# Kernel optimization log

Hardware: AMD Instinct MI355X
Metric: run time of the kernel (lower is better)

## Reference

```python
import jax, jax.numpy as jnp
import numpy as np

D_MODEL = 512
NHEAD = 8
HEAD_DIM = D_MODEL // NHEAD
SEQ = 4096
BATCH = 2
BASE = 10000.0


def rope_cache(seq_len, dim):
    inv_freq = 1.0 / (BASE ** (jnp.arange(0, dim, 2, dtype=jnp.float32) / dim))
    t = jnp.arange(seq_len, dtype=jnp.float32)
    freqs = jnp.einsum('i,j->ij', t, inv_freq)          # [S, dim/2]
    emb = jnp.concatenate([freqs, freqs], axis=-1)       # [S, dim]
    return jnp.cos(emb), jnp.sin(emb)


def rotate_half(x):
    h = x.shape[-1] // 2
    return jnp.concatenate([-x[..., h:], x[..., :h]], axis=-1)


def setup_inputs() -> dict:
    key = jax.random.key(0)
    ks = jax.random.split(key, 9)
    s = 1.0 / np.sqrt(D_MODEL)
    x = jax.random.normal(ks[0], (BATCH, SEQ, D_MODEL), dtype=jnp.float32)
    Wq = jax.random.uniform(ks[1], (D_MODEL, D_MODEL), jnp.float32, -s, s)
    bq = jax.random.uniform(ks[2], (D_MODEL,), jnp.float32, -s, s)
    Wk = jax.random.uniform(ks[3], (D_MODEL, D_MODEL), jnp.float32, -s, s)
    bk = jax.random.uniform(ks[4], (D_MODEL,), jnp.float32, -s, s)
    Wv = jax.random.uniform(ks[5], (D_MODEL, D_MODEL), jnp.float32, -s, s)
    bv = jax.random.uniform(ks[6], (D_MODEL,), jnp.float32, -s, s)
    Wo = jax.random.uniform(ks[7], (D_MODEL, D_MODEL), jnp.float32, -s, s)
    bo = jax.random.uniform(ks[8], (D_MODEL,), jnp.float32, -s, s)
    # causal mask: True where attention is disallowed (j > i)
    mask = jnp.triu(jnp.ones((SEQ, SEQ), dtype=bool), k=1)
    return {"x": x, "mask": mask, "Wq": Wq, "bq": bq, "Wk": Wk, "bk": bk,
            "Wv": Wv, "bv": bv, "Wo": Wo, "bo": bo}


def reference(x, mask, Wq, bq, Wk, bk, Wv, bv, Wo, bo):
    B, S, _ = x.shape
    def proj(W, b):
        y = x @ W.T + b
        return y.reshape(B, S, NHEAD, HEAD_DIM).transpose(0, 2, 1, 3)  # [B,H,S,D]
    q = proj(Wq, bq)
    k = proj(Wk, bk)
    v = proj(Wv, bv)
    cos, sin = rope_cache(S, HEAD_DIM)                    # [S, D]
    cos = cos[None, None]; sin = sin[None, None]
    q = q * cos + rotate_half(q) * sin
    k = k * cos + rotate_half(k) * sin
    scale = HEAD_DIM ** -0.5
    attn = jnp.einsum('bhid,bhjd->bhij', q, k) * scale    # [B,H,S,S]
    attn = jnp.where(mask[None, None], -jnp.inf, attn)
    attn = jax.nn.softmax(attn, axis=-1)
    out = jnp.einsum('bhij,bhjd->bhid', attn, v)          # [B,H,S,D]
    out = out.transpose(0, 2, 1, 3).reshape(B, S, D_MODEL)
    return out @ Wo.T + bo
```

## Files before the change

### kernel.cpp

```cpp
#include <hip/hip_runtime.h>
#include <hip/hip_bf16.h>

#define SEQLEN 4096
#define DMODEL 512
#define NHEADS 8

typedef short short8 __attribute__((ext_vector_type(8)));
typedef float f32x4  __attribute__((ext_vector_type(4)));
typedef float f32x16 __attribute__((ext_vector_type(16)));

__device__ __forceinline__ unsigned short f2bf(float f) {
    union { float f; unsigned u; } v; v.f = f;
    unsigned r = v.u + 0x7fffu + ((v.u >> 16) & 1u);
    return (unsigned short)(r >> 16);
}
__device__ __forceinline__ float exp2v(float x) {
    float r; asm("v_exp_f32 %0, %1" : "=v"(r) : "v"(x)); return r;
}
__device__ __forceinline__ unsigned cvtpk(float lo, float hi) {
    unsigned r; asm("v_cvt_pk_bf16_f32 %0, %1, %2" : "=v"(r) : "v"(lo), "v"(hi)); return r;
}
__device__ __forceinline__ void gload16(const void* g, void* l) {
    __builtin_amdgcn_global_load_lds(
        (const __attribute__((address_space(1))) void*)g,
        (__attribute__((address_space(3))) void*)l, 16, 0, 0);
}

__global__ __launch_bounds__(256)
void prep_kernel(const float* __restrict__ x,
                 const float* __restrict__ Wq, const float* __restrict__ Wk,
                 const float* __restrict__ Wv, const float* __restrict__ Wo,
                 unsigned short* __restrict__ xb, unsigned short* __restrict__ Wcat,
                 float* __restrict__ ct, float* __restrict__ st) {
    const int gid = blockIdx.x, tid = threadIdx.x;
    if (gid < 4096) {
        int i = gid * 1024 + tid * 4;
        float4 v = *reinterpret_cast<const float4*>(x + i);
        ushort4 o; o.x = f2bf(v.x); o.y = f2bf(v.y); o.z = f2bf(v.z); o.w = f2bf(v.w);
        *reinterpret_cast<ushort4*>(xb + i) = o;
    } else if (gid < 5120) {
        int i = (gid - 4096) * 1024 + tid * 4;
        int z = i >> 18;
        const float* W = (z == 0) ? Wq : (z == 1) ? Wk : (z == 2) ? Wv : Wo;
        int j = i & 262143;
        float4 v = *reinterpret_cast<const float4*>(W + j);
        ushort4 o; o.x = f2bf(v.x); o.y = f2bf(v.y); o.z = f2bf(v.z); o.w = f2bf(v.w);
        *reinterpret_cast<ushort4*>(Wcat + i) = o;
    } else {
        int idx = (gid - 5120) * 256 + tid;
        int s = idx >> 5, f = idx & 31;
        float inv = powf(10000.0f, -(float)f * (1.0f / 32.0f));
        float a = (float)s * inv;
        ct[idx] = cosf(a); st[idx] = sinf(a);
    }
}

template<int MODE>
__global__ __launch_bounds__(256)
void gemm_kernel(const unsigned short* __restrict__ A,
                 const unsigned short* __restrict__ W,
                 const float* __restrict__ bq,
                 const float* __restrict__ bk,
                 const float* __restrict__ bv,
                 const float* __restrict__ ctab,
                 const float* __restrict__ stab,
                 unsigned short* __restrict__ Qb,
                 unsigned short* __restrict__ Kb,
                 unsigned short* __restrict__ Vb,
                 float* __restrict__ Fout)
{
    constexpr int K = 512;
    constexpr int NT = (MODE == 0) ? 12 : 4;
    __shared__ __align__(16) unsigned short a_sh[2][128 * 32];
    __shared__ __align__(16) unsigned short b_sh[2][128 * 32];

    const int bid = blockIdx.x;
    const int bm = bid / NT, bn = bid % NT;
    const int tid = threadIdx.x;
    const int w = tid >> 6, l = tid & 63;
    const int g = l >> 4, l15 = l & 15;
    const int wr = w >> 1, wc = w & 1;

    const int sr0 = tid >> 2;
    const int swzc = (tid & 3) ^ ((sr0 >> 1) & 3);
    const unsigned wbase = (unsigned)(tid & 0xC0) * 16;
    const unsigned short* arow = A + (size_t)(bm * 128 + sr0) * K + swzc * 8;
    const unsigned short* brow = W + (size_t)(bn * 128 + sr0) * K + swzc * 8;

    f32x4 acc[4][4];
    #pragma unroll
    for (int p = 0; p < 4; ++p)
        #pragma unroll
        for (int q = 0; q < 4; ++q)
            acc[p][q] = (f32x4){0.f, 0.f, 0.f, 0.f};

    auto stage = [&](int buf, int k0) {
        char* ab = (char*)a_sh[buf];
        char* bb2 = (char*)b_sh[buf];
        #pragma unroll
        for (int rr = 0; rr < 2; ++rr)
            gload16(arow + (size_t)rr * 64 * K + k0, ab + rr * 4096 + wbase);
        #pragma unroll
        for (int rr = 0; rr < 2; ++rr)
            gload16(brow + (size_t)rr * 64 * K + k0, bb2 + rr * 4096 + wbase);
    };

    stage(0, 0);
    asm volatile("s_waitcnt vmcnt(0)" ::: "memory");
    __syncthreads();

    for (int ks = 0; ks < 16; ++ks) {
        const int buf = ks & 1;
        if (ks < 15) stage(buf ^ 1, (ks + 1) * 32);

        const char* ab = (const char*)a_sh[buf];
        const char* bb2 = (const char*)b_sh[buf];
        short8 af[4], bf[4];
        #pragma unroll
        for (int mt = 0; mt < 4; ++mt) {
            int r = wr * 64 + mt * 16 + l15;
            int ofs = (r * 64 + g * 16) ^ (((r >> 1) & 3) << 4);
            af[mt] = *reinterpret_cast<const short8*>(ab + ofs);
        }
        #pragma unroll
        for (int nt = 0; nt < 4; ++nt) {
            int r = wc * 64 + nt * 16 + l15;
            int ofs = (r * 64 + g * 16) ^ (((r >> 1) & 3) << 4);
            bf[nt] = *reinterpret_cast<const short8*>(bb2 + ofs);
        }
        __builtin_amdgcn_s_setprio(1);
        #pragma unroll
        for (int mt = 0; mt < 4; ++mt)
            #pragma unroll
            for (int nt = 0; nt < 4; ++nt)
                acc[mt][nt] = __builtin_amdgcn_mfma_f32_16x16x32_bf16(af[mt], bf[nt], acc[mt][nt], 0, 0, 0);
        __builtin_amdgcn_s_setprio(0);

        asm volatile("s_waitcnt vmcnt(0)" ::: "memory");
        __syncthreads();
    }

    const int m_base = bm * 128 + wr * 64;

    if (MODE == 1) {
        const int n_base = bn * 128 + wc * 64;
        #pragma unroll
        for (int mt = 0; mt < 4; ++mt)
            for (int nt = 0; nt < 4; ++nt) {
                int n = n_base + nt * 16 + l15;
                float bb = bq[n];
                #pragma unroll
                for (int i = 0; i < 4; ++i) {
                    int m = m_base + mt * 16 + g * 4 + i;
                    Fout[(size_t)m * 512 + n] = acc[mt][nt][i] + bb;
                }
            }
    } else {
        const int z = bn >> 2;
        const int nc0 = (bn & 3) * 128 + wc * 64;
        const float* bias = (z == 0) ? bq : (z == 1) ? bk : bv;
        if (z < 2) {
            unsigned short* Y = z ? Kb : Qb;
            const float qsc = z ? 1.0f : 0.18033688011112042f;
            #pragma unroll
            for (int mt = 0; mt < 4; ++mt)
                for (int ntl = 0; ntl < 2; ++ntl) {
                    int hd0 = (ntl * 16 + l15) & 31;
                    int n0 = nc0 + ntl * 16 + l15;
                    float bb0 = bias[n0];
                    float bb1 = bias[n0 + 32];
                    #pragma unroll
                    for (int i = 0; i < 4; ++i) {
                        int m = m_base + mt * 16 + g * 4 + i;
                        int sidx = m & (SEQLEN - 1);
                        float cs = ctab[sidx * 32 + hd0];
                        float sn = stab[sidx * 32 + hd0];
                        float v0 = acc[mt][ntl][i] + bb0;
                        float v1 = acc[mt][ntl + 2][i] + bb1;
                        Y[(size_t)m * 512 + n0]      = f2bf((v0 * cs - v1 * sn) * qsc);
                        Y[(size_t)m * 512 + n0 + 32] = f2bf((v1 * cs + v0 * sn) * qsc);
                    }
                }
        } else {
            #pragma unroll
            for (int mt = 0; mt < 4; ++mt)
                for (int nt = 0; nt < 4; ++nt) {
                    int n0 = nc0 + nt * 16 + l15;
                    float bb = bias[n0];
                    #pragma unroll
                    for (int i = 0; i < 4; ++i) {
                        int m = m_base + mt * 16 + g * 4 + i;
                        Vb[(size_t)m * 512 + n0] = f2bf(acc[mt][nt][i] + bb);
                    }
                }
        }
    }
}

__global__ __launch_bounds__(256)
void vtrans_kernel(const unsigned short* __restrict__ V, unsigned short* __restrict__ Vt) {
    __shared__ __align__(16) unsigned short t_sh[64 * 64];
    const int bx = blockIdx.x;
    const int bh = bx >> 6, stile = bx & 63;
    const int b = bh >> 3, h = bh & 7;
    const int tid = threadIdx.x;
    const int s0 = stile * 64;
    #pragma unroll
    for (int it = 0; it < 2; ++it) {
        int idx = it * 256 + tid;
        int s = idx >> 3, cb = idx & 7;
        short8 v = *reinterpret_cast<const short8*>(V + (size_t)(b * 4096 + s0 + s) * 512 + h * 64 + cb * 8);
        int ofs = (s * 128 + cb * 16) ^ ((s & 7) << 4);
        *reinterpret_cast<short8*>(reinterpret_cast<char*>(t_sh) + ofs) = v;
    }
    __syncthreads();
    #pragma unroll
    for (int it = 0; it < 2; ++it) {
        int idx = it * 256 + tid;
        int d = idx >> 3, sb = idx & 7;
        union { unsigned short u[8]; short8 s8; } o;
        #pragma unroll
        for (int j = 0; j < 8; ++j) {
            int s = sb * 8 + j;
            int ofs = (s * 128 + d * 2) ^ ((s & 7) << 4);
            o.u[j] = *reinterpret_cast<const unsigned short*>(reinterpret_cast<const char*>(t_sh) + ofs);
        }
        *reinterpret_cast<short8*>(Vt + ((size_t)(bh * 64 + d)) * SEQLEN + s0 + sb * 8) = o.s8;
    }
}

template<int SPLIT>
__global__ __launch_bounds__(256)
void attn_kernel(const unsigned short* __restrict__ Qg,
                 const unsigned short* __restrict__ Kg,
                 const unsigned short* __restrict__ Vt,
                 unsigned short* __restrict__ O,
                 float* __restrict__ Opt,
                 float* __restrict__ Ml)
{
    __shared__ __align__(16) unsigned short k_sh[2][64 * 64];
    __shared__ __align__(16) unsigned short v_sh[2][64 * 64];

    const int bx = blockIdx.x;
    int bh, qb, sp;
    if (SPLIT) {
        const int qbi = bx >> 5;
        qb = 31 - qbi;
        bh = (bx & 31) >> 1;
        sp = bx & 1;
    } else {
        bh = bx & 15; qb = 31 - (bx >> 4); sp = 0;
    }
    const int t0 = SPLIT ? sp * (qb + 1) : 0;
    const int t1 = SPLIT ? t0 + qb + 1 : 2 * qb + 2;

    const int b = bh >> 3, hh = bh & 7;
    const int tid = threadIdx.x;
    const int w = tid >> 6, l = tid & 63;
    const int l31 = l & 31, h = l >> 5;

    const size_t qkbase = (size_t)b * SEQLEN * DMODEL + hh * 64;
    const unsigned short* Vrow = Vt + (size_t)bh * 64 * SEQLEN;

    const int r0 = tid >> 3, cb0 = tid & 7;
    const int scs = cb0 ^ (r0 & 7);
    const unsigned short* ksrc0 = Kg + qkbase + (size_t)r0 * DMODEL + scs * 8;
    const unsigned short* vsrc0 = Vrow + (size_t)r0 * SEQLEN + scs * 8;

    const int swz = (l31 & 7) << 4;
    const int td = 2 * qb + (w >> 1);
    const int tlimit = td + 1;
    const int qg = qb * 128 + w * 32 + l31;

    short8 qf[4];
    const unsigned short* qrow = Qg + qkbase + (size_t)qg * DMODEL;
    #pragma unroll
    for (int kk = 0; kk < 4; ++kk)
        qf[kk] = *reinterpret_cast<const short8*>(qrow + kk * 16 + h * 8);

    f32x16 oa0, oa1;
    #pragma unroll
    for (int i = 0; i < 16; ++i) { oa0[i] = 0.f; oa1[i] = 0.f; }
    float mrun = -3.0e38f, lrun = 0.f;

    auto stage = [&](int buf, int t) {
        char* kb = (char*)k_sh[buf];
        char* vb = (char*)v_sh[buf];
        const unsigned short* kp = ksrc0 + (size_t)t * 64 * DMODEL;
        const unsigned short* vp = vsrc0 + t * 64;
        gload16(kp,                     kb + tid * 16);
        gload16(kp + 32 * DMODEL,       kb + 4096 + tid * 16);
        gload16(vp,                     vb + tid * 16);
        gload16(vp + 32 * SEQLEN,       vb + 4096 + tid * 16);
    };

    stage(t0 & 1, t0);
    asm volatile("s_waitcnt vmcnt(0)" ::: "memory");
    __syncthreads();

    for (int t = t0; t < t1; ++t) {
        const int buf = t & 1;
        if (t + 1 < t1) stage(buf ^ 1, t + 1);

        if (t < tlimit) {
            const char* kb = (const char*)k_sh[buf];
            const char* vb = (const char*)v_sh[buf];

            f32x16 st0, st1;
            #pragma unroll
            for (int i = 0; i < 16; ++i) { st0[i] = 0.f; st1[i] = 0.f; }
            __builtin_amdgcn_s_setprio(1);
            #pragma unroll
            for (int kk = 0; kk < 4; ++kk) {
                short8 kf0 = *reinterpret_cast<const short8*>(kb + l31 * 128 + ((kk * 32 + h * 16) ^ swz));
                short8 kf1 = *reinterpret_cast<const short8*>(kb + (32 + l31) * 128 + ((kk * 32 + h * 16) ^ swz));
                st0 = __builtin_amdgcn_mfma_f32_32x32x16_bf16(kf0, qf[kk], st0, 0, 0, 0);
                st1 = __builtin_amdgcn_mfma_f32_32x32x16_bf16(kf1, qf[kk], st1, 0, 0, 0);
            }
            __builtin_amdgcn_s_setprio(0);

            if (t == td) {
                #pragma unroll
                for (int r = 0; r < 16; ++r) {
                    int rp = (r & 3) + 8 * (r >> 2) + 4 * h;
                    int kv0 = t * 64 + rp;
                    if (kv0 > qg)      st0[r] = -3.0e38f;
                    if (kv0 + 32 > qg) st1[r] = -3.0e38f;
                }
            }

            float pm = st0[0];
            #pragma unroll
            for (int r = 1; r < 16; ++r) pm = fmaxf(pm, st0[r]);
            #pragma unroll
            for (int r = 0; r < 16; ++r) pm = fmaxf(pm, st1[r]);
            pm = fmaxf(pm, __shfl_xor(pm, 32));
            float mn = mrun;
            if (__any(pm > mrun + 8.0f)) {
                mn = fmaxf(mrun, pm);
                float al = exp2v(mrun - mn);
                mrun = mn;
                lrun *= al;
                #pragma unroll
                for (int r = 0; r < 16; ++r) { oa0[r] *= al; oa1[r] *= al; }
            }
            float s = 0.f;
            #pragma unroll
            for (int r = 0; r < 16; ++r) { float p = exp2v(st0[r] - mn); st0[r] = p; s += p; }
            #pragma unroll
            for (int r = 0; r < 16; ++r) { float p = exp2v(st1[r] - mn); st1[r] = p; s += p; }
            s += __shfl_xor(s, 32);
            lrun += s;

            __builtin_amdgcn_s_setprio(1);
            #pragma unroll
            for (int bb = 0; bb < 4; ++bb) {
                const int rb = (bb & 1) * 8;
                float p0, p1, p2, p3, p4, p5, p6, p7;
                if (bb < 2) {
                    p0 = st0[rb + 0]; p1 = st0[rb + 1]; p2 = st0[rb + 2]; p3 = st0[rb + 3];
                    p4 = st0[rb + 4]; p5 = st0[rb + 5]; p6 = st0[rb + 6]; p7 = st0[rb + 7];
                } else {
                    p0 = st1[rb + 0]; p1 = st1[rb + 1]; p2 = st1[rb + 2]; p3 = st1[rb + 3];
                    p4 = st1[rb + 4]; p5 = st1[rb + 5]; p6 = st1[rb + 6]; p7 = st1[rb + 7];
                }
                unsigned pk0 = cvtpk(p0, p1);
                unsigned pk1 = cvtpk(p2, p3);
                unsigned pk2 = cvtpk(p4, p5);
                unsigned pk3 = cvtpk(p6, p7);
                unsigned sx0 = (unsigned)__shfl_xor((int)pk0, 32);
                unsigned sx1 = (unsigned)__shfl_xor((int)pk1, 32);
                unsigned sx2 = (unsigned)__shfl_xor((int)pk2, 32);
                unsigned sx3 = (unsigned)__shfl_xor((int)pk3, 32);
                union { unsigned u[4]; short8 s8; } pw;
                pw.u[0] = h ? sx2 : pk0;
                pw.u[1] = h ? sx3 : pk1;
                pw.u[2] = h ? pk2 : sx0;
                pw.u[3] = h ? pk3 : sx1;

                short8 vf0 = *reinterpret_cast<const short8*>(vb + l31 * 128 + ((bb * 32 + h * 16) ^ swz));
                short8 vf1 = *reinterpret_cast<const short8*>(vb + (32 + l31) * 128 + ((bb * 32 + h * 16) ^ swz));
                oa0 = __builtin_amdgcn_mfma_f32_32x32x16_bf16(vf0, pw.s8, oa0, 0, 0, 0);
                oa1 = __builtin_amdgcn_mfma_f32_32x32x16_bf16(vf1, pw.s8, oa1, 0, 0, 0);
            }
            __builtin_amdgcn_s_setprio(0);
        }

        asm volatile("s_waitcnt vmcnt(0)" ::: "memory");
        __syncthreads();
    }

    if (SPLIT) {
        *reinterpret_cast<float2*>(Ml + ((size_t)(sp * 16 + bh) * 4096 + qg) * 2) =
            make_float2(mrun, lrun);
        float* opbase = Opt + (size_t)(sp * 16 + bh) * 64 * 4096;
        #pragma unroll
        for (int r = 0; r < 16; r += 2) {
            int d0 = (r & 3) + 8 * (r >> 2) + 4 * h;
            opbase[(size_t)d0 * 4096 + qg]        = oa0[r];
            opbase[(size_t)(d0 + 1) * 4096 + qg]  = oa0[r + 1];
            opbase[(size_t)(d0 + 32) * 4096 + qg] = oa1[r];
            opbase[(size_t)(d0 + 33) * 4096 + qg] = oa1[r + 1];
        }
    } else {
        float inv = 1.0f / lrun;
        unsigned short* orow = O + qkbase + (size_t)qg * DMODEL;
        #pragma unroll
        for (int r = 0; r < 16; r += 2) {
            int d0 = (r & 3) + 8 * (r >> 2) + 4 * h;
            *reinterpret_cast<unsigned*>(orow + d0)      = cvtpk(oa0[r] * inv, oa0[r + 1] * inv);
            *reinterpret_cast<unsigned*>(orow + 32 + d0) = cvtpk(oa1[r] * inv, oa1[r + 1] * inv);
        }
    }
}

__global__ __launch_bounds__(256)
void combine_kernel(const float* __restrict__ Opt, const float* __restrict__ Ml,
                    unsigned short* __restrict__ O) {
    __shared__ float a0_sh[64], a1_sh[64];
    __shared__ unsigned short o_sh[64][72];
    const int bx = blockIdx.x;
    const int bh = bx >> 6, qt = bx & 63;
    const int b = bh >> 3, hh = bh & 7;
    const int q0 = qt * 64;
    const int tid = threadIdx.x;

    if (tid < 64) {
        int q = q0 + tid;
        float2 ml0 = *reinterpret_cast<const float2*>(Ml + ((size_t)bh * 4096 + q) * 2);
        float2 ml1 = *reinterpret_cast<const float2*>(Ml + ((size_t)(16 + bh) * 4096 + q) * 2);
        float m = fmaxf(ml0.x, ml1.x);
        float a0 = exp2v(ml0.x - m), a1 = exp2v(ml1.x - m);
        float inv = 1.0f / (a0 * ml0.y + a1 * ml1.y);
        a0_sh[tid] = a0 * inv;
        a1_sh[tid] = a1 * inv;
    }
    __syncthreads();

    const int d = tid >> 2, q4 = (tid & 3) * 16;
    const float* p0 = Opt + ((size_t)bh * 64 + d) * 4096 + q0 + q4;
    const float* p1 = Opt + ((size_t)(16 + bh) * 64 + d) * 4096 + q0 + q4;
    #pragma unroll
    for (int j = 0; j < 16; j += 4) {
        float4 v0 = *reinterpret_cast<const float4*>(p0 + j);
        float4 v1 = *reinterpret_cast<const float4*>(p1 + j);
        int q = q4 + j;
        o_sh[q + 0][d] = f2bf(a0_sh[q + 0] * v0.x + a1_sh[q + 0] * v1.x);
        o_sh[q + 1][d] = f2bf(a0_sh[q + 1] * v0.y + a1_sh[q + 1] * v1.y);
        o_sh[q + 2][d] = f2bf(a0_sh[q + 2] * v0.z + a1_sh[q + 2] * v1.z);
        o_sh[q + 3][d] = f2bf(a0_sh[q + 3] * v0.w + a1_sh[q + 3] * v1.w);
    }
    __syncthreads();

    const int qw = tid >> 2, dc = (tid & 3) * 16;
    unsigned short* orow = O + ((size_t)(b * 4096 + q0 + qw)) * 512 + hh * 64 + dc;
    #pragma unroll
    for (int j = 0; j < 2; ++j) {
        union { ushort4 h4[2]; short8 s8; } u;
        u.h4[0] = *reinterpret_cast<const ushort4*>(&o_sh[qw][dc + j * 8]);
        u.h4[1] = *reinterpret_cast<const ushort4*>(&o_sh[qw][dc + j * 8 + 4]);
        *reinterpret_cast<short8*>(orow + j * 8) = u.s8;
    }
}

extern "C" void kernel_launch(void* const* d_in, const int* in_sizes, int n_in,
                              void* d_out, int out_size, void* d_ws, size_t ws_size,
                              hipStream_t stream) {
    const float* x  = (const float*)d_in[0];
    const float* Wq = (const float*)d_in[2];
    const float* bq = (const float*)d_in[3];
    const float* Wk = (const float*)d_in[4];
    const float* bk = (const float*)d_in[5];
    const float* Wv = (const float*)d_in[6];
    const float* bv = (const float*)d_in[7];
    const float* Wo = (const float*)d_in[8];
    const float* bo = (const float*)d_in[9];
    float* out = (float*)d_out;

    const int MD = 8192 * 512;
    const int WD = 512 * 512;
    unsigned short* ws  = (unsigned short*)d_ws;
    unsigned short* xb  = ws;
    unsigned short* Qb  = xb + MD;
    unsigned short* Kb  = Qb + MD;
    unsigned short* Vb  = Kb + MD;
    unsigned short* Ob  = Vb + MD;
    unsigned short* Wcat = Ob + MD;
    float* ctab = (float*)(Wcat + 4 * WD);
    float* stab = ctab + SEQLEN * 32;
    unsigned short* Vt = xb;
    float* Opt = (float*)((char*)d_ws + 45088768ull);
    float* Ml  = (float*)((char*)d_ws + 78643200ull);
    const size_t NEED = 79691776ull;
    const bool split = (ws_size >= NEED);

    prep_kernel<<<5632, 256, 0, stream>>>(x, Wq, Wk, Wv, Wo, xb, Wcat, ctab, stab);

    gemm_kernel<0><<<dim3(64 * 12), 256, 0, stream>>>(
        xb, Wcat, bq, bk, bv, ctab, stab, Qb, Kb, Vb, nullptr);

    vtrans_kernel<<<1024, 256, 0, stream>>>(Vb, Vt);

    if (split) {
        attn_kernel<1><<<dim3(1024), 256, 0, stream>>>(Qb, Kb, Vt, nullptr, Opt, Ml);
        combine_kernel<<<dim3(1024), 256, 0, stream>>>(Opt, Ml, Ob);
    } else {
        attn_kernel<0><<<dim3(512), 256, 0, stream>>>(Qb, Kb, Vt, Ob, nullptr, nullptr);
    }

    gemm_kernel<1><<<dim3(64 * 4), 256, 0, stream>>>(
        Ob, Wcat + 3 * WD, bo, nullptr, nullptr, nullptr, nullptr,
        nullptr, nullptr, nullptr, out);
}
```

Baseline: 245.5 us.

## Triple-buffer GEMM and attention loads, swizzle GEMM blocks, use permlane32 swaps

Both the projection GEMM and the attention kernel move from double to triple-buffered LDS staging. Loads are issued two tiles ahead and the loop waits with vmcnt(4) instead of draining every load before each barrier. The GEMM also remaps block IDs in groups of eight, likely to improve L2 locality, and the attention softmax uses tree reductions plus permlane32_swap in place of ds-based shuffles for the max, sum and P repacking. This costs more LDS per block, which may reduce occupancy, and issues redundant final-tile loads so the vmcnt accounting stays uniform.

```diff
diff --git a/kernel.cpp b/kernel.cpp
--- a/kernel.cpp
+++ b/kernel.cpp
@@ -8,6 +8,7 @@
 typedef short short8 __attribute__((ext_vector_type(8)));
 typedef float f32x4  __attribute__((ext_vector_type(4)));
 typedef float f32x16 __attribute__((ext_vector_type(16)));
+typedef int   int2v  __attribute__((ext_vector_type(2)));
 
 __device__ __forceinline__ unsigned short f2bf(float f) {
     union { float f; unsigned u; } v; v.f = f;
@@ -19,6 +20,9 @@
 }
 __device__ __forceinline__ unsigned cvtpk(float lo, float hi) {
     unsigned r; asm("v_cvt_pk_bf16_f32 %0, %1, %2" : "=v"(r) : "v"(lo), "v"(hi)); return r;
+}
+__device__ __forceinline__ int2v pl32(int a, int b) {
+    return __builtin_amdgcn_permlane32_swap(a, b, false, false);
 }
 __device__ __forceinline__ void gload16(const void* g, void* l) {
     __builtin_amdgcn_global_load_lds(
@@ -71,10 +75,12 @@
 {
     constexpr int K = 512;
     constexpr int NT = (MODE == 0) ? 12 : 4;
-    __shared__ __align__(16) unsigned short a_sh[2][128 * 32];
-    __shared__ __align__(16) unsigned short b_sh[2][128 * 32];
-
-    const int bid = blockIdx.x;
+    constexpr int CPX = (MODE == 0) ? 96 : 32;
+    __shared__ __align__(16) unsigned short a_sh[3][128 * 32];
+    __shared__ __align__(16) unsigned short b_sh[3][128 * 32];
+
+    const int raw = blockIdx.x;
+    const int bid = (raw & 7) * CPX + (raw >> 3);
     const int bm = bid / NT, bn = bid % NT;
     const int tid = threadIdx.x;
     const int w = tid >> 6, l = tid & 63;
@@ -97,24 +103,24 @@
     auto stage = [&](int buf, int k0) {
         char* ab = (char*)a_sh[buf];
         char* bb2 = (char*)b_sh[buf];
-        #pragma unroll
-        for (int rr = 0; rr < 2; ++rr)
-            gload16(arow + (size_t)rr * 64 * K + k0, ab + rr * 4096 + wbase);
-        #pragma unroll
-        for (int rr = 0; rr < 2; ++rr)
-            gload16(brow + (size_t)rr * 64 * K + k0, bb2 + rr * 4096 + wbase);
+        gload16(arow + k0,                      ab + wbase);
+        gload16(arow + (size_t)64 * K + k0,     ab + 4096 + wbase);
+        gload16(brow + k0,                      bb2 + wbase);
+        gload16(brow + (size_t)64 * K + k0,     bb2 + 4096 + wbase);
     };
 
     stage(0, 0);
-    asm volatile("s_waitcnt vmcnt(0)" ::: "memory");
-    __syncthreads();
-
+    stage(1, 32);
+    asm volatile("s_waitcnt vmcnt(4)" ::: "memory");
+    __builtin_amdgcn_s_barrier();
+
+    int cb = 0;
     for (int ks = 0; ks < 16; ++ks) {
-        const int buf = ks & 1;
-        if (ks < 15) stage(buf ^ 1, (ks + 1) * 32);
-
-        const char* ab = (const char*)a_sh[buf];
-        const char* bb2 = (const char*)b_sh[buf];
+        int pb = cb + 2; if (pb >= 3) pb -= 3;
+        stage(pb, (ks + 2 < 16) ? (ks + 2) * 32 : 480);
+
+        const char* ab = (const char*)a_sh[cb];
+        const char* bb2 = (const char*)b_sh[cb];
         short8 af[4], bf[4];
         #pragma unroll
         for (int mt = 0; mt < 4; ++mt) {
@@ -136,8 +142,9 @@
                 acc[mt][nt] = __builtin_amdgcn_mfma_f32_16x16x32_bf16(af[mt], bf[nt], acc[mt][nt], 0, 0, 0);
         __builtin_amdgcn_s_setprio(0);
 
-        asm volatile("s_waitcnt vmcnt(0)" ::: "memory");
-        __syncthreads();
+        asm volatile("s_waitcnt vmcnt(4)" ::: "memory");
+        __builtin_amdgcn_s_barrier();
+        cb = (cb == 2) ? 0 : cb + 1;
     }
 
     const int m_base = bm * 128 + wr * 64;
@@ -238,8 +245,8 @@
                  float* __restrict__ Opt,
                  float* __restrict__ Ml)
 {
-    __shared__ __align__(16) unsigned short k_sh[2][64 * 64];
-    __shared__ __align__(16) unsigned short v_sh[2][64 * 64];
+    __shared__ __align__(16) unsigned short k_sh[3][64 * 64];
+    __shared__ __align__(16) unsigned short v_sh[3][64 * 64];
 
     const int bx = blockIdx.x;
     int bh, qb, sp;
@@ -294,17 +301,22 @@
         gload16(vp + 32 * SEQLEN,       vb + 4096 + tid * 16);
     };
 
-    stage(t0 & 1, t0);
-    asm volatile("s_waitcnt vmcnt(0)" ::: "memory");
-    __syncthreads();
+    int cb = t0 % 3;
+    stage(cb, t0);
+    {
+        int nb = cb + 1; if (nb >= 3) nb -= 3;
+        stage(nb, (t0 + 1 < t1) ? t0 + 1 : t1 - 1);
+    }
+    asm volatile("s_waitcnt vmcnt(4)" ::: "memory");
+    __builtin_amdgcn_s_barrier();
 
     for (int t = t0; t < t1; ++t) {
-        const int buf = t & 1;
-        if (t + 1 < t1) stage(buf ^ 1, t + 1);
+        int pb = cb + 2; if (pb >= 3) pb -= 3;
+        stage(pb, (t + 2 < t1) ? t + 2 : t1 - 1);
 
         if (t < tlimit) {
-            const char* kb = (const char*)k_sh[buf];
-            const char* vb = (const char*)v_sh[buf];
+            const char* kb = (const char*)k_sh[cb];
+            const char* vb = (const char*)v_sh[cb];
 
             f32x16 st0, st1;
             #pragma unroll
@@ -329,12 +341,16 @@
                 }
             }
 
-            float pm = st0[0];
-            #pragma unroll
-            for (int r = 1; r < 16; ++r) pm = fmaxf(pm, st0[r]);
-            #pragma unroll
-            for (int r = 0; r < 16; ++r) pm = fmaxf(pm, st1[r]);
-            pm = fmaxf(pm, __shfl_xor(pm, 32));
+            float mx[16];
+            #pragma unroll
+            for (int r = 0; r < 16; ++r) mx[r] = fmaxf(st0[r], st1[r]);
+            #pragma unroll
+            for (int str = 8; str >= 1; str >>= 1)
+                #pragma unroll
+                for (int r = 0; r < str; ++r) mx[r] = fmaxf(mx[r], mx[r + str]);
+            int2v rp2 = pl32(__float_as_int(mx[0]), __float_as_int(mx[0]));
+            float pm = fmaxf(__int_as_float(rp2[0]), __int_as_float(rp2[1]));
+
             float mn = mrun;
             if (__any(pm > mrun + 8.0f)) {
                 mn = fmaxf(mrun, pm);
@@ -344,13 +360,19 @@
                 #pragma unroll
                 for (int r = 0; r < 16; ++r) { oa0[r] *= al; oa1[r] *= al; }
             }
-            float s = 0.f;
-            #pragma unroll
-            for (int r = 0; r < 16; ++r) { float p = exp2v(st0[r] - mn); st0[r] = p; s += p; }
-            #pragma unroll
-            for (int r = 0; r < 16; ++r) { float p = exp2v(st1[r] - mn); st1[r] = p; s += p; }
-            s += __shfl_xor(s, 32);
-            lrun += s;
+            #pragma unroll
+            for (int r = 0; r < 16; ++r) st0[r] = exp2v(st0[r] - mn);
+            #pragma unroll
+            for (int r = 0; r < 16; ++r) st1[r] = exp2v(st1[r] - mn);
+            float sm[16];
+            #pragma unroll
+            for (int r = 0; r < 16; ++r) sm[r] = st0[r] + st1[r];
+            #pragma unroll
+            for (int str = 8; str >= 1; str >>= 1)
+                #pragma unroll
+                for (int r = 0; r < str; ++r) sm[r] += sm[r + str];
+            int2v rs2 = pl32(__float_as_int(sm[0]), __float_as_int(sm[0]));
+            lrun += __int_as_float(rs2[0]) + __int_as_float(rs2[1]);
 
             __builtin_amdgcn_s_setprio(1);
             #pragma unroll
@@ -364,19 +386,17 @@
                     p0 = st1[rb + 0]; p1 = st1[rb + 1]; p2 = st1[rb + 2]; p3 = st1[rb + 3];
                     p4 = st1[rb + 4]; p5 = st1[rb + 5]; p6 = st1[rb + 6]; p7 = st1[rb + 7];
                 }
-                unsigned pk0 = cvtpk(p0, p1);
-                unsigned pk1 = cvtpk(p2, p3);
-                unsigned pk2 = cvtpk(p4, p5);
-                unsigned pk3 = cvtpk(p6, p7);
-                unsigned sx0 = (unsigned)__shfl_xor((int)pk0, 32);
-                unsigned sx1 = (unsigned)__shfl_xor((int)pk1, 32);
-                unsigned sx2 = (unsigned)__shfl_xor((int)pk2, 32);
-                unsigned sx3 = (unsigned)__shfl_xor((int)pk3, 32);
-                union { unsigned u[4]; short8 s8; } pw;
-                pw.u[0] = h ? sx2 : pk0;
-                pw.u[1] = h ? sx3 : pk1;
-                pw.u[2] = h ? pk2 : sx0;
-                pw.u[3] = h ? pk3 : sx1;
+                int pk0 = (int)cvtpk(p0, p1);
+                int pk1 = (int)cvtpk(p2, p3);
+                int pk2 = (int)cvtpk(p4, p5);
+                int pk3 = (int)cvtpk(p6, p7);
+                int2v r02 = pl32(pk0, pk2);
+                int2v r13 = pl32(pk1, pk3);
+                union { int u[4]; short8 s8; } pw;
+                pw.u[0] = r02[0];
+                pw.u[1] = r13[0];
+                pw.u[2] = r02[1];
+                pw.u[3] = r13[1];
 
                 short8 vf0 = *reinterpret_cast<const short8*>(vb + l31 * 128 + ((bb * 32 + h * 16) ^ swz));
                 short8 vf1 = *reinterpret_cast<const short8*>(vb + (32 + l31) * 128 + ((bb * 32 + h * 16) ^ swz));
@@ -386,8 +406,9 @@
             __builtin_amdgcn_s_setprio(0);
         }
 
-        asm volatile("s_waitcnt vmcnt(0)" ::: "memory");
-        __syncthreads();
+        asm volatile("s_waitcnt vmcnt(4)" ::: "memory");
+        __builtin_amdgcn_s_barrier();
+        cb = (cb == 2) ? 0 : cb + 1;
     }
 
     if (SPLIT) {
```

After: 232.0 us. 5.5% less time.
